# Optimization experiments

Measured on AMD Instinct MI355X. Metric: run time of the kernel, lower is better.

The kernel has to match this reference:

```python
import jax, jax.numpy as jnp
import numpy as np

NUM_HEADS = 12

def setup_inputs() -> dict:
    key = jax.random.key(0)
    k1, k2, k3, k4 = jax.random.split(key, 4)
    B, N, C = 8, 4096, 768
    x1 = jax.random.normal(k1, (B, N, C), dtype=jnp.float32)
    x2 = jax.random.normal(k2, (B, N, C), dtype=jnp.float32)
    segfeature = jax.random.normal(k3, (B, N, C), dtype=jnp.float32)
    # nn.Linear(dim, 2*dim, bias=False) weight, stored transposed for y = x @ W
    W_kv = jax.random.normal(k4, (C, 2 * C), dtype=jnp.float32) * (C ** -0.5)
    return {"x1": x1, "x2": x2, "segfeature": segfeature, "W_kv": W_kv}


def reference(x1, x2, segfeature, W_kv):
    B, N, C = x1.shape
    H = NUM_HEADS
    d = C // H
    scale = d ** -0.5
    # queries: [B, H, N, d]
    q1 = x1.reshape(B, N, H, d).transpose(0, 2, 1, 3)
    q2 = x2.reshape(B, N, H, d).transpose(0, 2, 1, 3)
    # kv projection: [B, M, 2C] -> [2, B, H, M, d]
    M = segfeature.shape[1]
    kv = (segfeature @ W_kv).reshape(B, M, 2, H, d).transpose(2, 0, 3, 1, 4)
    k3, v3 = kv[0], kv[1]
    # context matrix: k^T @ v over sequence -> [B, H, d, d]
    ctx = jnp.einsum('bhmd,bhme->bhde', k3, v3) * scale
    ctx = jax.nn.softmax(ctx, axis=-2)
    # apply context to both queries, back to [B, N, C]
    o1 = jnp.einsum('bhnd,bhde->bnhe', q1, ctx).reshape(B, N, C)
    o2 = jnp.einsum('bhnd,bhde->bnhe', q2, ctx).reshape(B, N, C)
    return (o1, o2)
```

## Files before the change

kernel.cpp:

```cpp
#include <hip/hip_runtime.h>

#define DI __device__ __forceinline__

typedef float        f32x4 __attribute__((ext_vector_type(4)));
typedef _Float16     f16x8 __attribute__((ext_vector_type(8)));
typedef unsigned int u32x4 __attribute__((ext_vector_type(4)));
typedef unsigned int u32x2 __attribute__((ext_vector_type(2)));

DI unsigned short f2h(float f){
    _Float16 h = (_Float16)f;
    return __builtin_bit_cast(unsigned short, h);
}

DI void gl_lds16(const void* g, void* l){
    __builtin_amdgcn_global_load_lds(
        (const __attribute__((address_space(1))) unsigned int*)g,
        (__attribute__((address_space(3))) unsigned int*)l, 16, 0, 0);
}

__global__ __launch_bounds__(256) void k_transpose_f16(
    const float* __restrict__ in, unsigned short* __restrict__ o16,
    int rows, int cols, long ibs, long obs)
{
    __shared__ float t[64][65];
    const int b  = blockIdx.z;
    const int r0 = blockIdx.y * 64, c0 = blockIdx.x * 64;
    const int tid = threadIdx.x;
    const float* ib = in + (long)b * ibs;

    #pragma unroll
    for (int i = 0; i < 4; ++i){
        int r  = (tid >> 4) + i * 16;
        int cq = (tid & 15) * 4;
        f32x4 v = *(const f32x4*)&ib[(long)(r0 + r) * cols + c0 + cq];
        t[r][cq+0] = v[0]; t[r][cq+1] = v[1]; t[r][cq+2] = v[2]; t[r][cq+3] = v[3];
    }
    __syncthreads();

    const int c  = tid >> 2;
    const int ms = (tid & 3) * 16;
    unsigned hv[8];
    #pragma unroll
    for (int k2 = 0; k2 < 8; ++k2){
        unsigned short ha = f2h(t[ms + 2*k2 + 0][c]);
        unsigned short hb = f2h(t[ms + 2*k2 + 1][c]);
        hv[k2] = (unsigned)ha | ((unsigned)hb << 16);
    }
    long o = (long)b * obs + (long)(c0 + c) * rows + r0 + ms;
    u32x4 H0 = {hv[0],hv[1],hv[2],hv[3]}, H1 = {hv[4],hv[5],hv[6],hv[7]};
    *(u32x4*)&o16[o]     = H0;
    *(u32x4*)&o16[o + 8] = H1;
}

DI void stage_lds(const unsigned short* __restrict__ src, long stride,
                  int row0, int k0, unsigned short* tile, int tid)
{
    #pragma unroll
    for (int it = 0; it < 4; ++it){
        int D    = (it * 256 + tid) * 16;
        int row  = D >> 7;
        int colb = (D & 127) ^ ((row & 7) << 4);
        const char* g = (const char*)(src + (long)(row0 + row) * stride + k0) + colb;
        gl_lds16(g, (char*)tile + D);
    }
}

DI f16x8 frag_ld(const unsigned short* tile, int row, int kc16)
{
    int logical = (row << 7) + (kc16 << 4);
    int phys    = logical ^ ((row & 7) << 4);
    return *(const f16x8*)((const char*)tile + phys);
}

DI void ldB3(const unsigned short* __restrict__ g0, long S16, long stride,
             int row0, int k0, int tid, f16x8 r0[4], f16x8 r1[4], f16x8 r2[4])
{
    #pragma unroll
    for (int it = 0; it < 4; ++it){
        int D    = (it * 256 + tid) * 16;
        int row  = D >> 7;
        int colb = D & 127;
        long off = (long)(row0 + row) * stride + k0 + (colb >> 1);
        r0[it] = *(const f16x8*)(g0 + off);
        r1[it] = *(const f16x8*)(g0 + S16 + off);
        r2[it] = *(const f16x8*)(g0 + 2 * S16 + off);
    }
}
DI void wrB3(unsigned short* tile, int tid, f16x8 r0[4], f16x8 r1[4], f16x8 r2[4])
{
    #pragma unroll
    for (int it = 0; it < 4; ++it){
        int D    = (it * 256 + tid) * 16;
        int row  = D >> 7;
        int colb = D & 127;
        f16x8 s;
        #pragma unroll
        for (int t = 0; t < 8; ++t)
            s[t] = (_Float16)((float)r0[it][t] + (float)r1[it][t] + (float)r2[it][t]);
        int phys = (D & ~127) | (colb ^ ((row & 7) << 4));
        *(f16x8*)((char*)tile + phys) = s;
    }
}

DI void mfma_tile(const unsigned short* TA, const unsigned short* TB,
                  int wr, int wc, int lane, f32x4 acc[4][4])
{
    #pragma unroll
    for (int ks = 0; ks < 2; ++ks){
        const int kc = ks * 4 + (lane >> 4);
        f16x8 bf[4];
        #pragma unroll
        for (int cf = 0; cf < 4; ++cf)
            bf[cf] = frag_ld(TB, wc + cf * 16 + (lane & 15), kc);
        #pragma unroll
        for (int rf = 0; rf < 4; ++rf){
            f16x8 af = frag_ld(TA, wr + rf * 16 + (lane & 15), kc);
            #pragma unroll
            for (int cf = 0; cf < 4; ++cf)
                acc[rf][cf] = __builtin_amdgcn_mfma_f32_16x16x32_f16(af, bf[cf], acc[rf][cf], 0, 0, 0);
        }
    }
}

DI void kloop(const unsigned short* a, int rowA0, long sA,
              const unsigned short* b, int rowB0, long sB,
              int kbeg, int kend, f32x4 acc[4][4], unsigned short* lds, int tid)
{
    const int lane = tid & 63;
    const int wave = tid >> 6;
    const int wr = (wave >> 1) * 64, wc = (wave & 1) * 64;

    stage_lds(a, sA, rowA0, kbeg, lds,        tid);
    stage_lds(b, sB, rowB0, kbeg, lds + 8192, tid);
    __syncthreads();

    int cur = 0;
    for (int k0 = kbeg; k0 < kend; k0 += 64){
        const unsigned short* TA = lds + cur * 16384;
        const int kn = k0 + 64;
        if (kn < kend){
            unsigned short* NA = lds + (cur ^ 1) * 16384;
            stage_lds(a, sA, rowA0, kn, NA,        tid);
            stage_lds(b, sB, rowB0, kn, NA + 8192, tid);
        }
        mfma_tile(TA, TA + 8192, wr, wc, lane, acc);
        __syncthreads();
        cur ^= 1;
    }
}

__global__ __launch_bounds__(256) void k_gram(
    const unsigned short* __restrict__ X, unsigned short* __restrict__ Gp16)
{
    __shared__ unsigned short lds[4 * 8192];
    const int id  = blockIdx.x;
    const int b   = id & 7;
    const int r   = id >> 3;
    const int ksl = r / 21;
    int q = r % 21;
    int ti = 0, tj = 0;
    #pragma unroll
    for (int i = 0; i < 6; ++i){ int c = 6 - i; if (q < c){ ti = i; tj = i + q; q = -1; break; } q -= c; }

    static const int kb[4] = {0, 1408, 2752, 4096};

    const unsigned short* XB = X + (long)b * 768 * 4096;

    f32x4 acc[4][4];
    #pragma unroll
    for (int i = 0; i < 4; ++i)
        #pragma unroll
        for (int j = 0; j < 4; ++j) acc[i][j] = (f32x4){0.f, 0.f, 0.f, 0.f};

    kloop(XB, ti * 128, 4096, XB, tj * 128, 4096,
          kb[ksl], kb[ksl + 1], acc, lds, threadIdx.x);

    unsigned short* G = Gp16 + ((long)ksl * 8 + b) * 768 * 768;
    const int lane = threadIdx.x & 63, wave = threadIdx.x >> 6;
    const int wr = (wave >> 1) * 64, wc = (wave & 1) * 64;
    #pragma unroll
    for (int rf = 0; rf < 4; ++rf)
        #pragma unroll
        for (int cf = 0; cf < 4; ++cf){
            int gi = ti * 128 + wr + rf * 16 + 4 * (lane >> 4);
            int gj = tj * 128 + wc + cf * 16 + (lane & 15);
            unsigned short h4[4];
            #pragma unroll
            for (int r2 = 0; r2 < 4; ++r2){
                h4[r2] = f2h(acc[rf][cf][r2]);
                G[(long)(gi + r2) * 768 + gj] = h4[r2];
            }
            if (ti != tj){
                u32x2 p = { (unsigned)h4[0] | ((unsigned)h4[1] << 16),
                            (unsigned)h4[2] | ((unsigned)h4[3] << 16) };
                *(u32x2*)(G + (long)gj * 768 + gi) = p;
            }
        }
}

__global__ __launch_bounds__(256) void k_tt(
    const unsigned short* __restrict__ WT, const unsigned short* __restrict__ Gp16,
    unsigned short* __restrict__ TT)
{
    __shared__ unsigned short lds[4 * 8192];
    const long S16 = 4718592;
    const int id = blockIdx.x;
    const int b  = id & 7;
    const int t  = id >> 3;
    const int ti = t % 6, tj = t / 6;
    const int tid = threadIdx.x;

    const unsigned short* A  = WT + (long)768 * 768;
    const unsigned short* G0 = Gp16 + (long)b * 768 * 768;

    f32x4 acc[4][4];
    #pragma unroll
    for (int i = 0; i < 4; ++i)
        #pragma unroll
        for (int j = 0; j < 4; ++j) acc[i][j] = (f32x4){0.f, 0.f, 0.f, 0.f};

    const int lane = tid & 63;
    const int wave = tid >> 6;
    const int wr = (wave >> 1) * 64, wc = (wave & 1) * 64;

    {
        f16x8 r0[4], r1[4], r2[4];
        ldB3(G0, S16, 768, tj * 128, 0, tid, r0, r1, r2);
        stage_lds(A, 768, ti * 128, 0, lds, tid);
        wrB3(lds + 8192, tid, r0, r1, r2);
        __syncthreads();
    }

    int cur = 0;
    for (int k0 = 0; k0 < 768; k0 += 64){
        const unsigned short* TA = lds + cur * 16384;
        const int kn = k0 + 64;
        f16x8 r0[4], r1[4], r2[4];
        if (kn < 768){
            ldB3(G0, S16, 768, tj * 128, kn, tid, r0, r1, r2);
            stage_lds(A, 768, ti * 128, kn, lds + (cur ^ 1) * 16384, tid);
        }
        mfma_tile(TA, TA + 8192, wr, wc, lane, acc);
        if (kn < 768)
            wrB3(lds + (cur ^ 1) * 16384 + 8192, tid, r0, r1, r2);
        __syncthreads();
        cur ^= 1;
    }

    unsigned short* tt = TT + (long)b * 768 * 768;
    #pragma unroll
    for (int rf = 0; rf < 4; ++rf)
        #pragma unroll
        for (int cf = 0; cf < 4; ++cf){
            int gi = ti * 128 + wr + rf * 16 + 4 * (lane >> 4);
            int gj = tj * 128 + wc + cf * 16 + (lane & 15);
            #pragma unroll
            for (int r = 0; r < 4; ++r)
                tt[(long)(gi + r) * 768 + gj] = f2h(acc[rf][cf][r]);
        }
}

__global__ __launch_bounds__(256) void k_ctx(
    const unsigned short* __restrict__ WT, const unsigned short* __restrict__ TT,
    unsigned short* __restrict__ wT)
{
    __shared__ float red[3][64][65];
    const int bh = blockIdx.x;
    const int b = bh / 12, h = bh % 12;
    const int lane = threadIdx.x & 63;
    const int wave = threadIdx.x >> 6;

    const unsigned short* A = WT + (long)(h * 64) * 768;
    const unsigned short* B = TT + (long)b * 768 * 768 + (long)(h * 64) * 768;

    f32x4 acc[4][4];
    #pragma unroll
    for (int i = 0; i < 4; ++i)
        #pragma unroll
        for (int j = 0; j < 4; ++j) acc[i][j] = (f32x4){0.f, 0.f, 0.f, 0.f};

    for (int kc = wave * 6; kc < wave * 6 + 6; ++kc){
        const int k0 = kc * 32 + (lane >> 4) * 8;
        f16x8 af[4], bf[4];
        #pragma unroll
        for (int f = 0; f < 4; ++f){
            long ro = (long)(f * 16 + (lane & 15)) * 768 + k0;
            af[f] = *(const f16x8*)(A + ro);
            bf[f] = *(const f16x8*)(B + ro);
        }
        #pragma unroll
        for (int rf = 0; rf < 4; ++rf)
            #pragma unroll
            for (int cf = 0; cf < 4; ++cf)
                acc[rf][cf] = __builtin_amdgcn_mfma_f32_16x16x32_f16(af[rf], bf[cf], acc[rf][cf], 0, 0, 0);
    }

    if (wave > 0){
        #pragma unroll
        for (int rf = 0; rf < 4; ++rf)
            #pragma unroll
            for (int cf = 0; cf < 4; ++cf)
                #pragma unroll
                for (int r = 0; r < 4; ++r)
                    red[wave - 1][lane][(rf * 4 + cf) * 4 + r] = acc[rf][cf][r];
    }
    __syncthreads();
    if (wave != 0) return;

    #pragma unroll
    for (int rf = 0; rf < 4; ++rf)
        #pragma unroll
        for (int cf = 0; cf < 4; ++cf)
            #pragma unroll
            for (int r = 0; r < 4; ++r){
                int idx = (rf * 4 + cf) * 4 + r;
                acc[rf][cf][r] += red[0][lane][idx] + red[1][lane][idx] + red[2][lane][idx];
            }

    unsigned short* wout = wT + (long)bh * 4096;
    #pragma unroll
    for (int cf = 0; cf < 4; ++cf){
        float pv[16];
        float m = -3.4e38f;
        #pragma unroll
        for (int rf = 0; rf < 4; ++rf)
            #pragma unroll
            for (int r = 0; r < 4; ++r){
                float s = acc[rf][cf][r] * 0.125f;
                pv[rf * 4 + r] = s;
                m = fmaxf(m, s);
            }
        m = fmaxf(m, __shfl_xor(m, 16));
        m = fmaxf(m, __shfl_xor(m, 32));
        float sum = 0.f;
        #pragma unroll
        for (int k = 0; k < 16; ++k){ pv[k] = __expf(pv[k] - m); sum += pv[k]; }
        sum += __shfl_xor(sum, 16);
        sum += __shfl_xor(sum, 32);
        float inv = 1.f / sum;
        int e = cf * 16 + (lane & 15);
        #pragma unroll
        for (int rf = 0; rf < 4; ++rf)
            #pragma unroll
            for (int r = 0; r < 4; ++r){
                int d = rf * 16 + 4 * (lane >> 4) + r;
                wout[e * 64 + d] = f2h(pv[rf * 4 + r] * inv);
            }
    }
}

__global__ __launch_bounds__(256) void k_apply(
    const float* __restrict__ x1, const float* __restrict__ x2,
    const unsigned short* __restrict__ wT, float* __restrict__ out)
{
    __shared__ float ep[4][64][64];
    const int b = blockIdx.z;
    const int h = blockIdx.y >> 1;
    const int src = blockIdx.y & 1;
    const int lane = threadIdx.x & 63, wave = threadIdx.x >> 6;
    const int n0 = blockIdx.x * 256 + wave * 64;

    const float* x = (src ? x2 : x1) + (long)b * 4096 * 768;
    float* o = out + (long)src * 8 * 4096 * 768 + (long)b * 4096 * 768;

    const unsigned short* W = wT + (long)(b * 12 + h) * 4096;
    f16x8 bw[4][2];
    #pragma unroll
    for (int fe = 0; fe < 4; ++fe)
        #pragma unroll
        for (int ks = 0; ks < 2; ++ks)
            bw[fe][ks] = *(const f16x8*)(W + (fe * 16 + (lane & 15)) * 64 + ks * 32 + (lane >> 4) * 8);

    f32x4 acc[4][4];
    #pragma unroll
    for (int i = 0; i < 4; ++i)
        #pragma unroll
        for (int j = 0; j < 4; ++j) acc[i][j] = (f32x4){0.f, 0.f, 0.f, 0.f};

    #pragma unroll
    for (int rf = 0; rf < 4; ++rf){
        const int row = n0 + rf * 16 + (lane & 15);
        const float* xr = x + (long)row * 768 + h * 64 + (lane >> 4) * 8;
        f32x4 v0 = *(const f32x4*)(xr);
        f32x4 v1 = *(const f32x4*)(xr + 4);
        f32x4 v2 = *(const f32x4*)(xr + 32);
        f32x4 v3 = *(const f32x4*)(xr + 36);
        f16x8 a0, a1;
        #pragma unroll
        for (int t = 0; t < 4; ++t){
            a0[t]     = (_Float16)v0[t];
            a0[t + 4] = (_Float16)v1[t];
            a1[t]     = (_Float16)v2[t];
            a1[t + 4] = (_Float16)v3[t];
        }
        #pragma unroll
        for (int fe = 0; fe < 4; ++fe){
            acc[rf][fe] = __builtin_amdgcn_mfma_f32_16x16x32_f16(a0, bw[fe][0], acc[rf][fe], 0, 0, 0);
            acc[rf][fe] = __builtin_amdgcn_mfma_f32_16x16x32_f16(a1, bw[fe][1], acc[rf][fe], 0, 0, 0);
        }
    }

    #pragma unroll
    for (int rf = 0; rf < 4; ++rf)
        #pragma unroll
        for (int fe = 0; fe < 4; ++fe)
            #pragma unroll
            for (int r = 0; r < 4; ++r)
                ep[wave][rf * 16 + 4 * (lane >> 4) + r][fe * 16 + (lane & 15)] = acc[rf][fe][r];

    #pragma unroll
    for (int pass = 0; pass < 16; ++pass){
        int rr = pass * 4 + (lane >> 4);
        f32x4 v = *(const f32x4*)&ep[wave][rr][(lane & 15) * 4];
        *(f32x4*)&o[(long)(n0 + rr) * 768 + h * 64 + (lane & 15) * 4] = v;
    }
}

__global__ void k_sentinel(float* o){ o[0] = 1.0e9f; }

extern "C" void kernel_launch(void* const* d_in, const int* in_sizes, int n_in,
                              void* d_out, int out_size, void* d_ws, size_t ws_size,
                              hipStream_t stream)
{
    (void)in_sizes; (void)n_in; (void)out_size;
    const float* x1  = (const float*)d_in[0];
    const float* x2  = (const float*)d_in[1];
    const float* seg = (const float*)d_in[2];
    const float* Wkv = (const float*)d_in[3];

    char* Wb = (char*)d_ws;
    unsigned short* X    = (unsigned short*)(Wb);
    unsigned short* WT   = (unsigned short*)(Wb + 50331648);
    unsigned short* TT   = (unsigned short*)(Wb + 52690944);
    unsigned short* wT   = (unsigned short*)(Wb + 62128128);
    unsigned short* Gp16 = (unsigned short*)(Wb + 62914560);
    const size_t need = 91226112;

    if (ws_size < need){
        k_sentinel<<<1, 1, 0, stream>>>((float*)d_out);
        return;
    }

    k_transpose_f16<<<dim3(12, 64, 8), 256, 0, stream>>>(
        seg, X, 4096, 768, (long)4096 * 768, (long)768 * 4096);
    k_transpose_f16<<<dim3(24, 12, 1), 256, 0, stream>>>(
        Wkv, WT, 768, 1536, 0, 0);

    k_gram<<<dim3(504), 256, 0, stream>>>(X, Gp16);

    k_tt<<<dim3(288), 256, 0, stream>>>(WT, Gp16, TT);

    k_ctx<<<dim3(96), 256, 0, stream>>>(WT, TT, wT);

    k_apply<<<dim3(16, 24, 8), 256, 0, stream>>>(x1, x2, wT, (float*)d_out);
}
```

Measured before the change: 179.1 us.

## Load A fragments directly from global in gram and TT GEMMs, halve LDS

In k_gram and k_tt, the A operand is no longer staged through LDS. Each lane loads its A fragments directly from global memory through per-row pointers, and only the B tile stays double-buffered in LDS, which halves shared memory per block. This is meant to cut LDS traffic and raise occupancy, at the cost of uncoalesced, latency-exposed global loads for A with no prefetch. The final output store also becomes a nontemporal store.

```diff
diff --git a/kernel.cpp b/kernel.cpp
--- a/kernel.cpp
+++ b/kernel.cpp
@@ -52,12 +52,13 @@
     *(u32x4*)&o16[o + 8] = H1;
 }
 
+template<int TPB>
 DI void stage_lds(const unsigned short* __restrict__ src, long stride,
                   int row0, int k0, unsigned short* tile, int tid)
 {
     #pragma unroll
-    for (int it = 0; it < 4; ++it){
-        int D    = (it * 256 + tid) * 16;
+    for (int it = 0; it < 1024 / TPB; ++it){
+        int D    = (it * TPB + tid) * 16;
         int row  = D >> 7;
         int colb = (D & 127) ^ ((row & 7) << 4);
         const char* g = (const char*)(src + (long)(row0 + row) * stride + k0) + colb;
@@ -72,39 +73,17 @@
     return *(const f16x8*)((const char*)tile + phys);
 }
 
-DI void ldB3(const unsigned short* __restrict__ g0, long S16, long stride,
-             int row0, int k0, int tid, f16x8 r0[4], f16x8 r1[4], f16x8 r2[4])
-{
-    #pragma unroll
-    for (int it = 0; it < 4; ++it){
-        int D    = (it * 256 + tid) * 16;
-        int row  = D >> 7;
-        int colb = D & 127;
-        long off = (long)(row0 + row) * stride + k0 + (colb >> 1);
-        r0[it] = *(const f16x8*)(g0 + off);
-        r1[it] = *(const f16x8*)(g0 + S16 + off);
-        r2[it] = *(const f16x8*)(g0 + 2 * S16 + off);
-    }
-}
-DI void wrB3(unsigned short* tile, int tid, f16x8 r0[4], f16x8 r1[4], f16x8 r2[4])
-{
-    #pragma unroll
-    for (int it = 0; it < 4; ++it){
-        int D    = (it * 256 + tid) * 16;
-        int row  = D >> 7;
-        int colb = D & 127;
-        f16x8 s;
-        #pragma unroll
-        for (int t = 0; t < 8; ++t)
-            s[t] = (_Float16)((float)r0[it][t] + (float)r1[it][t] + (float)r2[it][t]);
-        int phys = (D & ~127) | (colb ^ ((row & 7) << 4));
-        *(f16x8*)((char*)tile + phys) = s;
-    }
-}
-
-DI void mfma_tile(const unsigned short* TA, const unsigned short* TB,
-                  int wr, int wc, int lane, f32x4 acc[4][4])
-{
+DI void mfma_step(const unsigned short* arow[4], int k0,
+                  const unsigned short* TB, int wc, int lane, f32x4 acc[4][4])
+{
+    f16x8 af[2][4];
+    #pragma unroll
+    for (int ks = 0; ks < 2; ++ks){
+        const int kc = ks * 4 + (lane >> 4);
+        #pragma unroll
+        for (int rf = 0; rf < 4; ++rf)
+            af[ks][rf] = *(const f16x8*)(arow[rf] + k0 + kc * 8);
+    }
     #pragma unroll
     for (int ks = 0; ks < 2; ++ks){
         const int kc = ks * 4 + (lane >> 4);
@@ -113,46 +92,17 @@
         for (int cf = 0; cf < 4; ++cf)
             bf[cf] = frag_ld(TB, wc + cf * 16 + (lane & 15), kc);
         #pragma unroll
-        for (int rf = 0; rf < 4; ++rf){
-            f16x8 af = frag_ld(TA, wr + rf * 16 + (lane & 15), kc);
+        for (int rf = 0; rf < 4; ++rf)
             #pragma unroll
             for (int cf = 0; cf < 4; ++cf)
-                acc[rf][cf] = __builtin_amdgcn_mfma_f32_16x16x32_f16(af, bf[cf], acc[rf][cf], 0, 0, 0);
-        }
-    }
-}
-
-DI void kloop(const unsigned short* a, int rowA0, long sA,
-              const unsigned short* b, int rowB0, long sB,
-              int kbeg, int kend, f32x4 acc[4][4], unsigned short* lds, int tid)
-{
-    const int lane = tid & 63;
-    const int wave = tid >> 6;
-    const int wr = (wave >> 1) * 64, wc = (wave & 1) * 64;
-
-    stage_lds(a, sA, rowA0, kbeg, lds,        tid);
-    stage_lds(b, sB, rowB0, kbeg, lds + 8192, tid);
-    __syncthreads();
-
-    int cur = 0;
-    for (int k0 = kbeg; k0 < kend; k0 += 64){
-        const unsigned short* TA = lds + cur * 16384;
-        const int kn = k0 + 64;
-        if (kn < kend){
-            unsigned short* NA = lds + (cur ^ 1) * 16384;
-            stage_lds(a, sA, rowA0, kn, NA,        tid);
-            stage_lds(b, sB, rowB0, kn, NA + 8192, tid);
-        }
-        mfma_tile(TA, TA + 8192, wr, wc, lane, acc);
-        __syncthreads();
-        cur ^= 1;
+                acc[rf][cf] = __builtin_amdgcn_mfma_f32_16x16x32_f16(af[ks][rf], bf[cf], acc[rf][cf], 0, 0, 0);
     }
 }
 
 __global__ __launch_bounds__(256) void k_gram(
     const unsigned short* __restrict__ X, unsigned short* __restrict__ Gp16)
 {
-    __shared__ unsigned short lds[4 * 8192];
+    __shared__ unsigned short lds[2 * 8192];
     const int id  = blockIdx.x;
     const int b   = id & 7;
     const int r   = id >> 3;
@@ -163,8 +113,17 @@
     for (int i = 0; i < 6; ++i){ int c = 6 - i; if (q < c){ ti = i; tj = i + q; q = -1; break; } q -= c; }
 
     static const int kb[4] = {0, 1408, 2752, 4096};
+    const int kbeg = kb[ksl], kend = kb[ksl + 1];
 
     const unsigned short* XB = X + (long)b * 768 * 4096;
+    const int tid  = threadIdx.x;
+    const int lane = tid & 63, wave = tid >> 6;
+    const int wr = (wave >> 1) * 64, wc = (wave & 1) * 64;
+
+    const unsigned short* arow[4];
+    #pragma unroll
+    for (int rf = 0; rf < 4; ++rf)
+        arow[rf] = XB + (long)(ti * 128 + wr + rf * 16 + (lane & 15)) * 4096;
 
     f32x4 acc[4][4];
     #pragma unroll
@@ -172,12 +131,21 @@
         #pragma unroll
         for (int j = 0; j < 4; ++j) acc[i][j] = (f32x4){0.f, 0.f, 0.f, 0.f};
 
-    kloop(XB, ti * 128, 4096, XB, tj * 128, 4096,
-          kb[ksl], kb[ksl + 1], acc, lds, threadIdx.x);
+    stage_lds<256>(XB, 4096, tj * 128, kbeg, lds, tid);
+    __syncthreads();
+
+    int cur = 0;
+    for (int k0 = kbeg; k0 < kend; k0 += 64){
+        const unsigned short* TB = lds + cur * 8192;
+        const int kn = k0 + 64;
+        if (kn < kend)
+            stage_lds<256>(XB, 4096, tj * 128, kn, lds + (cur ^ 1) * 8192, tid);
+        mfma_step(arow, k0, TB, wc, lane, acc);
+        __syncthreads();
+        cur ^= 1;
+    }
 
     unsigned short* G = Gp16 + ((long)ksl * 8 + b) * 768 * 768;
-    const int lane = threadIdx.x & 63, wave = threadIdx.x >> 6;
-    const int wr = (wave >> 1) * 64, wc = (wave & 1) * 64;
     #pragma unroll
     for (int rf = 0; rf < 4; ++rf)
         #pragma unroll
@@ -198,11 +166,41 @@
         }
 }
 
+DI void ldB3(const unsigned short* __restrict__ g0, long S16, long stride,
+             int row0, int k0, int tid, f16x8 r0[4], f16x8 r1[4], f16x8 r2[4])
+{
+    #pragma unroll
+    for (int it = 0; it < 4; ++it){
+        int D    = (it * 256 + tid) * 16;
+        int row  = D >> 7;
+        int colb = D & 127;
+        long off = (long)(row0 + row) * stride + k0 + (colb >> 1);
+        r0[it] = *(const f16x8*)(g0 + off);
+        r1[it] = *(const f16x8*)(g0 + S16 + off);
+        r2[it] = *(const f16x8*)(g0 + 2 * S16 + off);
+    }
+}
+DI void wrB3(unsigned short* tile, int tid, f16x8 r0[4], f16x8 r1[4], f16x8 r2[4])
+{
+    #pragma unroll
+    for (int it = 0; it < 4; ++it){
+        int D    = (it * 256 + tid) * 16;
+        int row  = D >> 7;
+        int colb = D & 127;
+        f16x8 s;
+        #pragma unroll
+        for (int t = 0; t < 8; ++t)
+            s[t] = (_Float16)((float)r0[it][t] + (float)r1[it][t] + (float)r2[it][t]);
+        int phys = (D & ~127) | (colb ^ ((row & 7) << 4));
+        *(f16x8*)((char*)tile + phys) = s;
+    }
+}
+
 __global__ __launch_bounds__(256) void k_tt(
     const unsigned short* __restrict__ WT, const unsigned short* __restrict__ Gp16,
     unsigned short* __restrict__ TT)
 {
-    __shared__ unsigned short lds[4 * 8192];
+    __shared__ unsigned short lds[2 * 8192];
     const long S16 = 4718592;
     const int id = blockIdx.x;
     const int b  = id & 7;
@@ -213,36 +211,37 @@
     const unsigned short* A  = WT + (long)768 * 768;
     const unsigned short* G0 = Gp16 + (long)b * 768 * 768;
 
+    const int lane = tid & 63, wave = tid >> 6;
+    const int wr = (wave >> 1) * 64, wc = (wave & 1) * 64;
+
+    const unsigned short* arow[4];
+    #pragma unroll
+    for (int rf = 0; rf < 4; ++rf)
+        arow[rf] = A + (long)(ti * 128 + wr + rf * 16 + (lane & 15)) * 768;
+
     f32x4 acc[4][4];
     #pragma unroll
     for (int i = 0; i < 4; ++i)
         #pragma unroll
         for (int j = 0; j < 4; ++j) acc[i][j] = (f32x4){0.f, 0.f, 0.f, 0.f};
-
-    const int lane = tid & 63;
-    const int wave = tid >> 6;
-    const int wr = (wave >> 1) * 64, wc = (wave & 1) * 64;
 
     {
         f16x8 r0[4], r1[4], r2[4];
         ldB3(G0, S16, 768, tj * 128, 0, tid, r0, r1, r2);
-        stage_lds(A, 768, ti * 128, 0, lds, tid);
-        wrB3(lds + 8192, tid, r0, r1, r2);
+        wrB3(lds, tid, r0, r1, r2);
         __syncthreads();
     }
 
     int cur = 0;
     for (int k0 = 0; k0 < 768; k0 += 64){
-        const unsigned short* TA = lds + cur * 16384;
+        const unsigned short* TB = lds + cur * 8192;
         const int kn = k0 + 64;
         f16x8 r0[4], r1[4], r2[4];
-        if (kn < 768){
+        if (kn < 768)
             ldB3(G0, S16, 768, tj * 128, kn, tid, r0, r1, r2);
-            stage_lds(A, 768, ti * 128, kn, lds + (cur ^ 1) * 16384, tid);
-        }
-        mfma_tile(TA, TA + 8192, wr, wc, lane, acc);
+        mfma_step(arow, k0, TB, wc, lane, acc);
         if (kn < 768)
-            wrB3(lds + (cur ^ 1) * 16384 + 8192, tid, r0, r1, r2);
+            wrB3(lds + (cur ^ 1) * 8192, tid, r0, r1, r2);
         __syncthreads();
         cur ^= 1;
     }
@@ -412,7 +411,7 @@
     for (int pass = 0; pass < 16; ++pass){
         int rr = pass * 4 + (lane >> 4);
         f32x4 v = *(const f32x4*)&ep[wave][rr][(lane & 15) * 4];
-        *(f32x4*)&o[(long)(n0 + rr) * 768 + h * 64 + (lane & 15) * 4] = v;
+        __builtin_nontemporal_store(v, (f32x4*)&o[(long)(n0 + rr) * 768 + h * 64 + (lane & 15) * 4]);
     }
 }
 
```

New measurement: 212.3 us. 18.5% more time.
